# Kernel tuning notes

Hardware: AMD Instinct MI355X
Metric: run time of the kernel (lower is better)

Reference implementation:

```python
import jax, jax.numpy as jnp
import numpy as np

N_NODES = 100000


def _sage_conv(x, src, dst, Wl, Wr, b):
    # PyG SAGEConv (aggr='mean'): out = lin_l(mean_j x_j) + lin_r(x_i)
    deg = jax.ops.segment_sum(jnp.ones_like(src, dtype=x.dtype), dst, num_segments=N_NODES)
    agg = jax.ops.segment_sum(x[src], dst, num_segments=N_NODES)
    agg = agg / jnp.clip(deg, 1.0)[:, None]
    return agg @ Wl.T + x @ Wr.T + b


def setup_inputs() -> dict:
    key = jax.random.key(0)
    ks = jax.random.split(key, 16)
    N, E, ES = N_NODES, 1600000, 100000
    IN, H, D = 64, 128, 64

    def lin(k, out_c, in_c):
        s = 1.0 / np.sqrt(in_c)
        return jax.random.uniform(k, (out_c, in_c), jnp.float32, -s, s)

    inp = {
        "x": jax.random.normal(ks[0], (N, IN), jnp.float32),
        "edge_index": jax.random.randint(ks[1], (2, E), 0, N, jnp.int64),
        "edge_sample": jax.random.randint(ks[2], (2, ES), 0, N, jnp.int64),
        # SAGEConv 0: 64 -> 128
        "Wl0": lin(ks[3], H, IN), "Wr0": lin(ks[4], H, IN), "b0": jnp.zeros((H,), jnp.float32),
        # SAGEConv 1: 128 -> 128
        "Wl1": lin(ks[5], H, H), "Wr1": lin(ks[6], H, H), "b1": jnp.zeros((H,), jnp.float32),
        # SAGEConv 2: 128 -> 64
        "Wl2": lin(ks[7], D, H), "Wr2": lin(ks[8], D, H), "b2": jnp.zeros((D,), jnp.float32),
        # feature decoder MLP: 64 -> 128 -> 64
        "Wd1": lin(ks[9], H, D), "bd1": jnp.zeros((H,), jnp.float32),
        "Wd2": lin(ks[10], IN, H), "bd2": jnp.zeros((IN,), jnp.float32),
    }
    return inp


def reference(x, edge_index, edge_sample, Wl0, Wr0, b0, Wl1, Wr1, b1, Wl2, Wr2, b2, Wd1, bd1, Wd2, bd2):
    src, dst = edge_index[0], edge_index[1]
    # encoder (dropout = identity at inference)
    h = jax.nn.relu(_sage_conv(x, src, dst, Wl0, Wr0, b0))
    h = jax.nn.relu(_sage_conv(h, src, dst, Wl1, Wr1, b1))
    emb = _sage_conv(h, src, dst, Wl2, Wr2, b2)
    # feature decoder
    rec = jax.nn.relu(emb @ Wd1.T + bd1) @ Wd2.T + bd2
    # edge decoder: dot product
    edge_scores = jnp.sum(emb[edge_sample[0]] * emb[edge_sample[1]], axis=1)
    return emb, rec, edge_scores
```

## Files before the change

kernel.cpp:

```cpp
#include <hip/hip_runtime.h>

#define NN 100000
#define NBK 98
#define CHUNK 8192
typedef unsigned int uint;
typedef unsigned short ushort;

using f32x4 = __attribute__((ext_vector_type(4))) float;
using s16x8 = __attribute__((ext_vector_type(8))) short;

__device__ inline ushort f32_to_bf16(float f) {
  uint u = __float_as_uint(f);
  uint r = (u + 0x7FFFu + ((u >> 16) & 1u)) >> 16;
  return (ushort)r;
}
__device__ inline float bf16_to_f32(ushort h) {
  return __uint_as_float(((uint)h) << 16);
}

typedef __attribute__((address_space(1))) const unsigned int gas_u32;
typedef __attribute__((address_space(3))) unsigned int las_u32;
__device__ __forceinline__ void gld_lds16(const void* gp, void* lp) {
  __builtin_amdgcn_global_load_lds((gas_u32*)gp, (las_u32*)lp, 16, 0, 0);
}

struct P8 { const float* p[8]; };

__global__ void k_prep(const int* __restrict__ dst, uint* __restrict__ bcnt, int E, int NCB,
                       const float* __restrict__ x, ushort* __restrict__ xb, int n4, int NC,
                       P8 w, ushort* __restrict__ whi, int wtotal) {
  int b = blockIdx.x;
  int tid = threadIdx.x;
  if (b < NCB) {
    __shared__ uint hist[NBK];
    for (int i = tid; i < NBK; i += 256) hist[i] = 0;
    __syncthreads();
    int base = b * CHUNK;
    int lim = min(base + CHUNK, E);
    for (int e = base + tid; e < lim; e += 256) atomicAdd(&hist[(uint)dst[e] >> 10], 1u);
    __syncthreads();
    for (int i = tid; i < NBK; i += 256)
      if (hist[i]) atomicAdd(&bcnt[i], hist[i]);
  } else if (b < NCB + NC) {
    int i = (b - NCB) * 256 + tid;
    if (i < n4) {
      float4 v = ((const float4*)x)[i];
      uint2 o;
      o.x = (uint)f32_to_bf16(v.x) | ((uint)f32_to_bf16(v.y) << 16);
      o.y = (uint)f32_to_bf16(v.z) | ((uint)f32_to_bf16(v.w) << 16);
      ((uint2*)xb)[i] = o;
    }
  } else {
    int g = (b - NCB - NC) * 256 + tid;
    if (g < wtotal) {
      const int offs[8] = {0, 8192, 16384, 32768, 49152, 57344, 65536, 73728};
      int s = 0;
#pragma unroll
      for (int i = 1; i < 8; ++i) s += (g >= offs[i]);
      whi[g] = f32_to_bf16(w.p[s][g - offs[s]]);
    }
  }
}

__global__ void k_bscan(const uint* __restrict__ bcnt, uint* __restrict__ bbase,
                        uint* __restrict__ bcur, int* __restrict__ rp) {
  if (threadIdx.x == 0) {
    uint s = 0;
    for (int i = 0; i < NBK; ++i) {
      uint c = bcnt[i];
      bbase[i] = s;
      bcur[i] = s;
      s += c;
    }
    bbase[NBK] = s;
    rp[NN] = (int)s;
  }
}

__global__ void k_bscatter(const int* __restrict__ src, const int* __restrict__ dst,
                           uint* __restrict__ bcur, uint* __restrict__ packed, int E) {
  __shared__ uint hist[NBK], runbase[NBK], cur[NBK];
  int tid = threadIdx.x;
  for (int i = tid; i < NBK; i += 256) hist[i] = 0;
  __syncthreads();
  int base = blockIdx.x * CHUNK;
  int lim = min(base + CHUNK, E);
  for (int e = base + tid; e < lim; e += 256) atomicAdd(&hist[(uint)dst[e] >> 10], 1u);
  __syncthreads();
  for (int i = tid; i < NBK; i += 256) {
    runbase[i] = hist[i] ? atomicAdd(&bcur[i], hist[i]) : 0u;
    cur[i] = 0;
  }
  __syncthreads();
  for (int e = base + tid; e < lim; e += 256) {
    uint d = (uint)dst[e];
    uint s = (uint)src[e];
    uint bk = d >> 10;
    uint p = runbase[bk] + atomicAdd(&cur[bk], 1u);
    packed[p] = ((d & 1023u) << 20) | s;
  }
}

__global__ void k_build(const uint* __restrict__ bbase, const uint* __restrict__ packed,
                        int* __restrict__ rp, int* __restrict__ col) {
  __shared__ uint hist[1024];
  __shared__ uint ws[256];
  int b = blockIdx.x;
  int tid = threadIdx.x;
  uint lo = bbase[b], hi = bbase[b + 1];
#pragma unroll
  for (int i = 0; i < 4; ++i) hist[tid + i * 256] = 0;
  __syncthreads();
  for (uint e = lo + tid; e < hi; e += 256) atomicAdd(&hist[packed[e] >> 20], 1u);
  __syncthreads();
  uint v0 = hist[tid * 4], v1 = hist[tid * 4 + 1], v2 = hist[tid * 4 + 2], v3 = hist[tid * 4 + 3];
  ws[tid] = v0 + v1 + v2 + v3;
  __syncthreads();
  for (int off = 1; off < 256; off <<= 1) {
    uint add = (tid >= off) ? ws[tid - off] : 0u;
    __syncthreads();
    ws[tid] += add;
    __syncthreads();
  }
  uint ex = (tid > 0) ? ws[tid - 1] : 0u;
  hist[tid * 4] = ex;
  hist[tid * 4 + 1] = ex + v0;
  hist[tid * 4 + 2] = ex + v0 + v1;
  hist[tid * 4 + 3] = ex + v0 + v1 + v2;
  int nodeBase = b << 10;
#pragma unroll
  for (int i = 0; i < 4; ++i) {
    int node = nodeBase + tid * 4 + i;
    if (node < NN) rp[node] = (int)(lo + hist[tid * 4 + i]);
  }
  __syncthreads();
  for (uint e = lo + tid; e < hi; e += 256) {
    uint pk = packed[e];
    uint p = atomicAdd(&hist[pk >> 20], 1u);
    col[lo + p] = (int)(pk & 0xFFFFFu);
  }
}

#define ACC1(vv) { alo += __uint_as_float((vv) << 16); ahi += __uint_as_float((vv) & 0xffff0000u); }

template <int F, int MODE>
__global__ void k_agg(const ushort* __restrict__ x, const int* __restrict__ rp,
                      const int* __restrict__ col, const float* __restrict__ u,
                      float* __restrict__ of, ushort* __restrict__ ob, int n) {
  constexpr int RS = F / 2;
  int wave = (blockIdx.x * blockDim.x + threadIdx.x) >> 6;
  int lane = threadIdx.x & 63;
  int node, l;
  if (F == 128) { node = wave; l = lane; }
  else { node = wave * 2 + (lane >> 5); l = lane & 31; }
  if (node >= n) return;
  int beg = rp[node], end = rp[node + 1];
  int deg = end - beg;
  const uint* __restrict__ xu = (const uint*)x;
  float alo = 0.f, ahi = 0.f;
  int j = beg;
  for (; j + 8 <= end; j += 8) {
    int c0 = col[j], c1 = col[j + 1], c2 = col[j + 2], c3 = col[j + 3];
    int c4 = col[j + 4], c5 = col[j + 5], c6 = col[j + 6], c7 = col[j + 7];
    uint v0 = xu[(size_t)c0 * RS + l];
    uint v1 = xu[(size_t)c1 * RS + l];
    uint v2 = xu[(size_t)c2 * RS + l];
    uint v3 = xu[(size_t)c3 * RS + l];
    uint v4 = xu[(size_t)c4 * RS + l];
    uint v5 = xu[(size_t)c5 * RS + l];
    uint v6 = xu[(size_t)c6 * RS + l];
    uint v7 = xu[(size_t)c7 * RS + l];
    ACC1(v0) ACC1(v1) ACC1(v2) ACC1(v3) ACC1(v4) ACC1(v5) ACC1(v6) ACC1(v7)
  }
  if (j + 4 <= end) {
    int c0 = col[j], c1 = col[j + 1], c2 = col[j + 2], c3 = col[j + 3];
    uint v0 = xu[(size_t)c0 * RS + l];
    uint v1 = xu[(size_t)c1 * RS + l];
    uint v2 = xu[(size_t)c2 * RS + l];
    uint v3 = xu[(size_t)c3 * RS + l];
    ACC1(v0) ACC1(v1) ACC1(v2) ACC1(v3)
    j += 4;
  }
  for (; j < end; ++j) {
    uint v0 = xu[(size_t)col[j] * RS + l];
    ACC1(v0)
  }
  float inv = 1.0f / (float)(deg > 0 ? deg : 1);
  alo *= inv;
  ahi *= inv;
  if (MODE == 0) {
    ((uint*)ob)[(size_t)node * RS + l] = (uint)f32_to_bf16(alo) | ((uint)f32_to_bf16(ahi) << 16);
  } else {
    float2 uv = ((const float2*)u)[(size_t)node * RS + l];
    float e0 = alo + uv.x, e1 = ahi + uv.y;
    ((float2*)of)[(size_t)node * RS + l] = make_float2(e0, e1);
    ((uint*)ob)[(size_t)node * RS + l] = (uint)f32_to_bf16(e0) | ((uint)f32_to_bf16(e1) << 16);
  }
}

template <int K, int H, bool RELU, bool DUAL, int OUTM>
__global__ __launch_bounds__(256) void k_gemm(
    const ushort* __restrict__ A, const ushort* __restrict__ Wa,
    const ushort* __restrict__ B, const ushort* __restrict__ Wb,
    const float* __restrict__ bias,
    float* __restrict__ outf, ushort* __restrict__ outb, int n) {
  constexpr int BM = 128;
  constexpr int KT = 64;
  constexpr int NKT = K / KT;
  constexpr int MF = (H == 128) ? 4 : 2;
  constexpr int WCH = H / 32;
  __shared__ ushort As[BM * KT];
  __shared__ ushort Ws[H * KT];

  const int tid = threadIdx.x;
  const int lane = tid & 63;
  const int wid = tid >> 6;
  const int fr = lane & 15;
  const int fq = lane >> 4;
  const int blockRow = blockIdx.x * BM;
  const int rowBase = (H == 128) ? (wid >> 1) * 64 : wid * 32;
  const int colBase = (H == 128) ? (wid & 1) * 64 : 0;
  const int srow = lane >> 3;
  const int sslot = (lane & 7) ^ srow;
  const bool fullTile = (blockRow + BM <= n);

  f32x4 acc[MF][4];
#pragma unroll
  for (int mi = 0; mi < MF; ++mi)
#pragma unroll
    for (int ni = 0; ni < 4; ++ni) acc[mi][ni] = (f32x4){0.f, 0.f, 0.f, 0.f};

#pragma unroll
  for (int phase = 0; phase < (DUAL ? 2 : 1); ++phase) {
    const ushort* __restrict__ Ap = phase ? B : A;
    const ushort* __restrict__ Wp = phase ? Wb : Wa;
#pragma unroll
    for (int kt = 0; kt < NKT; ++kt) {
      const int ktb = kt * KT;
      __syncthreads();
      if (fullTile) {
#pragma unroll
        for (int i = 0; i < 4; ++i) {
          int r0 = (wid + i * 4) * 8;
          gld_lds16(Ap + (size_t)(blockRow + r0 + srow) * K + ktb + sslot * 8,
                    (char*)As + r0 * 128);
        }
#pragma unroll
        for (int i = 0; i < WCH; ++i) {
          int r0 = (wid + i * 4) * 8;
          if (WCH >= 4 || wid + i * 4 < WCH * 4)
            gld_lds16(Wp + (size_t)(r0 + srow) * K + ktb + sslot * 8,
                      (char*)Ws + r0 * 128);
        }
      } else {
        for (int c = tid; c < BM * 8; c += 256) {
          int r = c >> 3, kc = c & 7;
          int row = blockRow + r;
          uint4 v = make_uint4(0u, 0u, 0u, 0u);
          if (row < n) v = *(const uint4*)(Ap + (size_t)row * K + ktb + kc * 8);
          *(uint4*)((char*)As + r * 128 + ((kc * 16) ^ ((r & 7) << 4))) = v;
        }
        for (int c = tid; c < H * 8; c += 256) {
          int r = c >> 3, kc = c & 7;
          *(uint4*)((char*)Ws + r * 128 + ((kc * 16) ^ ((r & 7) << 4))) =
              *(const uint4*)(Wp + (size_t)r * K + ktb + kc * 8);
        }
      }
      __syncthreads();
#pragma unroll
      for (int ks = 0; ks < 2; ++ks) {
        const int kb = ks * 64 + fq * 16;
        s16x8 af[MF], wf[4];
#pragma unroll
        for (int mi = 0; mi < MF; ++mi) {
          int r = rowBase + mi * 16 + fr;
          af[mi] = *(const s16x8*)((const char*)As + r * 128 + (kb ^ ((r & 7) << 4)));
        }
#pragma unroll
        for (int ni = 0; ni < 4; ++ni) {
          int r = colBase + ni * 16 + fr;
          wf[ni] = *(const s16x8*)((const char*)Ws + r * 128 + (kb ^ ((r & 7) << 4)));
        }
#pragma unroll
        for (int mi = 0; mi < MF; ++mi)
#pragma unroll
          for (int ni = 0; ni < 4; ++ni)
            acc[mi][ni] = __builtin_amdgcn_mfma_f32_16x16x32_bf16(af[mi], wf[ni], acc[mi][ni], 0, 0, 0);
      }
    }
  }
#pragma unroll
  for (int mi = 0; mi < MF; ++mi) {
#pragma unroll
    for (int ni = 0; ni < 4; ++ni) {
#pragma unroll
      for (int r = 0; r < 4; ++r) {
        int row = blockRow + rowBase + mi * 16 + fq * 4 + r;
        int colI = colBase + ni * 16 + fr;
        if (row < n) {
          float v = acc[mi][ni][r];
          if (OUTM == 3) {
            if (colI < 64)
              outb[(size_t)row * 64 + colI] = f32_to_bf16(v);
            else
              outf[(size_t)row * 64 + (colI - 64)] = v + bias[colI - 64];
          } else {
            if (bias) v += bias[colI];
            if (RELU) v = fmaxf(v, 0.f);
            if (OUTM == 1) outf[(size_t)row * H + colI] = v;
            else outb[(size_t)row * H + colI] = f32_to_bf16(v);
          }
        }
      }
    }
  }
}

__global__ void k_dot(const float* __restrict__ emb, const int* __restrict__ ea,
                      const int* __restrict__ eb, float* __restrict__ out, int ne) {
  int hw = (blockIdx.x * blockDim.x + threadIdx.x) >> 5;
  int l = threadIdx.x & 31;
  if (hw >= ne) return;
  float2 a = ((const float2*)(emb + (size_t)ea[hw] * 64))[l];
  float2 b = ((const float2*)(emb + (size_t)eb[hw] * 64))[l];
  float v = a.x * b.x + a.y * b.y;
#pragma unroll
  for (int off = 16; off; off >>= 1) v += __shfl_xor(v, off, 64);
  if (l == 0) out[hw] = v;
}

extern "C" void kernel_launch(void* const* d_in, const int* in_sizes, int n_in,
                              void* d_out, int out_size, void* d_ws, size_t ws_size,
                              hipStream_t stream) {
  const float* x = (const float*)d_in[0];
  const int* ei = (const int*)d_in[1];
  const int* es = (const int*)d_in[2];
  const float* b0 = (const float*)d_in[5];
  const float* b1 = (const float*)d_in[8];
  const float* b2 = (const float*)d_in[11];
  const float* bd1 = (const float*)d_in[13];
  const float* bd2 = (const float*)d_in[15];

  const int E = in_sizes[1] / 2;
  const int ES = in_sizes[2] / 2;
  const int* srcv = ei;
  const int* dstv = ei + E;
  const int* ea = es;
  const int* eb = es + ES;

  char* wp = (char*)d_ws;
  auto alloc = [&](size_t bytes) {
    char* p = wp;
    wp += (bytes + 511) & ~(size_t)511;
    return p;
  };
  int* row_ptr = (int*)alloc((NN + 1) * sizeof(int));
  uint* bcnt = (uint*)alloc(NBK * sizeof(uint));
  uint* bbase = (uint*)alloc((NBK + 1) * sizeof(uint));
  uint* bcur = (uint*)alloc(NBK * sizeof(uint));
  uint* packed = (uint*)alloc((size_t)E * sizeof(uint));
  int* colv = (int*)alloc((size_t)E * sizeof(int));
  ushort* xb = (ushort*)alloc((size_t)NN * 64 * 2);
  ushort* aggb = (ushort*)alloc((size_t)NN * 128 * 2);
  ushort* h1b = (ushort*)alloc((size_t)NN * 128 * 2);
  ushort* h2b = (ushort*)alloc((size_t)NN * 128 * 2);
  float* uf = (float*)alloc((size_t)NN * 64 * 4);
  ushort* embb = (ushort*)alloc((size_t)NN * 64 * 2);
  ushort* Whb = (ushort*)alloc(81920 * 2);

  const int WO0 = 0, WO1 = 8192, WO2 = 16384, WO3 = 32768, WO4 = 49152,
            WO6 = 65536, WO7 = 73728;

  float* out_emb = (float*)d_out;
  float* out_rec = out_emb + (size_t)NN * 64;
  float* out_sc = out_rec + (size_t)NN * 64;

  hipMemsetAsync(bcnt, 0, NBK * sizeof(uint), stream);

  P8 wptrs;
  wptrs.p[0] = (const float*)d_in[3];  wptrs.p[1] = (const float*)d_in[4];
  wptrs.p[2] = (const float*)d_in[6];  wptrs.p[3] = (const float*)d_in[7];
  wptrs.p[4] = (const float*)d_in[9];  wptrs.p[5] = (const float*)d_in[10];
  wptrs.p[6] = (const float*)d_in[12]; wptrs.p[7] = (const float*)d_in[14];

  const int NCB = (E + CHUNK - 1) / CHUNK;
  const int n4 = NN * 64 / 4;
  const int NC = (n4 + 255) / 256;
  const int NS = (81920 + 255) / 256;
  k_prep<<<NCB + NC + NS, 256, 0, stream>>>(dstv, bcnt, E, NCB, x, xb, n4, NC,
                                            wptrs, Whb, 81920);
  k_bscan<<<1, 64, 0, stream>>>(bcnt, bbase, bcur, row_ptr);
  k_bscatter<<<NCB, 256, 0, stream>>>(srcv, dstv, bcur, packed, E);
  k_build<<<NBK, 256, 0, stream>>>(bbase, packed, row_ptr, colv);

  const int g64 = (NN + 7) / 8;
  const int g128a = (NN + 3) / 4;
  dim3 gg((NN + 127) / 128);

  k_agg<64, 0><<<g64, 256, 0, stream>>>(xb, row_ptr, colv, nullptr, nullptr, aggb, NN);
  k_gemm<64, 128, true, true, 0><<<gg, 256, 0, stream>>>(
      aggb, Whb + WO0, xb, Whb + WO1, b0, nullptr, h1b, NN);
  k_agg<128, 0><<<g128a, 256, 0, stream>>>(h1b, row_ptr, colv, nullptr, nullptr, aggb, NN);
  k_gemm<128, 128, true, true, 0><<<gg, 256, 0, stream>>>(
      aggb, Whb + WO2, h1b, Whb + WO3, b1, nullptr, h2b, NN);
  k_gemm<128, 128, false, false, 3><<<gg, 256, 0, stream>>>(
      h2b, Whb + WO4, nullptr, nullptr, b2, uf, aggb, NN);
  k_agg<64, 2><<<g64, 256, 0, stream>>>(aggb, row_ptr, colv, uf, out_emb, embb, NN);
  k_gemm<64, 128, true, false, 0><<<gg, 256, 0, stream>>>(
      embb, Whb + WO6, nullptr, nullptr, bd1, nullptr, h1b, NN);
  k_gemm<128, 64, false, false, 1><<<gg, 256, 0, stream>>>(
      h1b, Whb + WO7, nullptr, nullptr, bd2, out_rec, nullptr, NN);
  k_dot<<<(ES + 7) / 8, 256, 0, stream>>>(out_emb, ea, eb, out_sc, ES);
}
```

Before: 366.6 us.

## Fuse decoder MLP, load full-K GEMM tiles, precompute per-chunk scatter offsets

Three changes. The two decoder GEMMs are merged into one kernel that keeps the 128-wide hidden activation in LDS, so it is never written to and reread from global memory. The GEMM kernel now loads the whole K extent of A and W into LDS at once instead of looping over 64-wide K tiles, which removes per-tile barriers but uses more LDS per block. The bucket scatter reuses per-chunk histograms from the prep kernel plus a per-bucket scan, so it no longer recomputes histograms or issues global atomics; the cost is a serial scan over chunks in a single block.

```diff
diff --git a/kernel.cpp b/kernel.cpp
--- a/kernel.cpp
+++ b/kernel.cpp
@@ -26,7 +26,8 @@
 
 struct P8 { const float* p[8]; };
 
-__global__ void k_prep(const int* __restrict__ dst, uint* __restrict__ bcnt, int E, int NCB,
+__global__ void k_prep(const int* __restrict__ dst, uint* __restrict__ bcnt,
+                       uint* __restrict__ chunkCnt, int E, int NCB,
                        const float* __restrict__ x, ushort* __restrict__ xb, int n4, int NC,
                        P8 w, ushort* __restrict__ whi, int wtotal) {
   int b = blockIdx.x;
@@ -39,8 +40,11 @@
     int lim = min(base + CHUNK, E);
     for (int e = base + tid; e < lim; e += 256) atomicAdd(&hist[(uint)dst[e] >> 10], 1u);
     __syncthreads();
-    for (int i = tid; i < NBK; i += 256)
-      if (hist[i]) atomicAdd(&bcnt[i], hist[i]);
+    for (int i = tid; i < NBK; i += 256) {
+      uint h = hist[i];
+      chunkCnt[(size_t)b * NBK + i] = h;
+      if (h) atomicAdd(&bcnt[i], h);
+    }
   } else if (b < NCB + NC) {
     int i = (b - NCB) * 256 + tid;
     if (i < n4) {
@@ -63,40 +67,45 @@
 }
 
 __global__ void k_bscan(const uint* __restrict__ bcnt, uint* __restrict__ bbase,
-                        uint* __restrict__ bcur, int* __restrict__ rp) {
+                        int* __restrict__ rp, const uint* __restrict__ chunkCnt,
+                        uint* __restrict__ chunkBase, int NCB) {
+  __shared__ uint sbase[NBK + 1];
   if (threadIdx.x == 0) {
     uint s = 0;
     for (int i = 0; i < NBK; ++i) {
-      uint c = bcnt[i];
-      bbase[i] = s;
-      bcur[i] = s;
-      s += c;
-    }
-    bbase[NBK] = s;
+      sbase[i] = s;
+      s += bcnt[i];
+    }
+    sbase[NBK] = s;
     rp[NN] = (int)s;
+    for (int i = 0; i <= NBK; ++i) bbase[i] = sbase[i];
+  }
+  __syncthreads();
+  int bk = threadIdx.x;
+  if (bk < NBK) {
+    uint run = sbase[bk];
+    for (int c = 0; c < NCB; ++c) {
+      uint v = chunkCnt[(size_t)c * NBK + bk];
+      chunkBase[(size_t)c * NBK + bk] = run;
+      run += v;
+    }
   }
 }
 
 __global__ void k_bscatter(const int* __restrict__ src, const int* __restrict__ dst,
-                           uint* __restrict__ bcur, uint* __restrict__ packed, int E) {
-  __shared__ uint hist[NBK], runbase[NBK], cur[NBK];
+                           const uint* __restrict__ chunkBase, uint* __restrict__ packed, int E) {
+  __shared__ uint cur[NBK];
   int tid = threadIdx.x;
-  for (int i = tid; i < NBK; i += 256) hist[i] = 0;
-  __syncthreads();
-  int base = blockIdx.x * CHUNK;
+  int b = blockIdx.x;
+  for (int i = tid; i < NBK; i += 256) cur[i] = chunkBase[(size_t)b * NBK + i];
+  __syncthreads();
+  int base = b * CHUNK;
   int lim = min(base + CHUNK, E);
-  for (int e = base + tid; e < lim; e += 256) atomicAdd(&hist[(uint)dst[e] >> 10], 1u);
-  __syncthreads();
-  for (int i = tid; i < NBK; i += 256) {
-    runbase[i] = hist[i] ? atomicAdd(&bcur[i], hist[i]) : 0u;
-    cur[i] = 0;
-  }
-  __syncthreads();
   for (int e = base + tid; e < lim; e += 256) {
     uint d = (uint)dst[e];
     uint s = (uint)src[e];
     uint bk = d >> 10;
-    uint p = runbase[bk] + atomicAdd(&cur[bk], 1u);
+    uint p = atomicAdd(&cur[bk], 1u);
     packed[p] = ((d & 1023u) << 20) | s;
   }
 }
@@ -205,12 +214,14 @@
     const float* __restrict__ bias,
     float* __restrict__ outf, ushort* __restrict__ outb, int n) {
   constexpr int BM = 128;
-  constexpr int KT = 64;
-  constexpr int NKT = K / KT;
   constexpr int MF = (H == 128) ? 4 : 2;
-  constexpr int WCH = H / 32;
-  __shared__ ushort As[BM * KT];
-  __shared__ ushort Ws[H * KT];
+  constexpr int RB = 2 * K;
+  constexpr int SLOTS = K / 8;
+  constexpr int CR = 1024 / RB;
+  constexpr int ACH = BM * RB / 1024;
+  constexpr int WCHN = H * RB / 1024;
+  __shared__ ushort As[BM * K];
+  __shared__ ushort Ws[H * K];
 
   const int tid = threadIdx.x;
   const int lane = tid & 63;
@@ -220,8 +231,8 @@
   const int blockRow = blockIdx.x * BM;
   const int rowBase = (H == 128) ? (wid >> 1) * 64 : wid * 32;
   const int colBase = (H == 128) ? (wid & 1) * 64 : 0;
-  const int srow = lane >> 3;
-  const int sslot = (lane & 7) ^ srow;
+  const int srow = lane / SLOTS;
+  const int sl = lane % SLOTS;
   const bool fullTile = (blockRow + BM <= n);
 
   f32x4 acc[MF][4];
@@ -234,59 +245,54 @@
   for (int phase = 0; phase < (DUAL ? 2 : 1); ++phase) {
     const ushort* __restrict__ Ap = phase ? B : A;
     const ushort* __restrict__ Wp = phase ? Wb : Wa;
-#pragma unroll
-    for (int kt = 0; kt < NKT; ++kt) {
-      const int ktb = kt * KT;
-      __syncthreads();
-      if (fullTile) {
-#pragma unroll
-        for (int i = 0; i < 4; ++i) {
-          int r0 = (wid + i * 4) * 8;
-          gld_lds16(Ap + (size_t)(blockRow + r0 + srow) * K + ktb + sslot * 8,
-                    (char*)As + r0 * 128);
-        }
-#pragma unroll
-        for (int i = 0; i < WCH; ++i) {
-          int r0 = (wid + i * 4) * 8;
-          if (WCH >= 4 || wid + i * 4 < WCH * 4)
-            gld_lds16(Wp + (size_t)(r0 + srow) * K + ktb + sslot * 8,
-                      (char*)Ws + r0 * 128);
-        }
-      } else {
-        for (int c = tid; c < BM * 8; c += 256) {
-          int r = c >> 3, kc = c & 7;
-          int row = blockRow + r;
-          uint4 v = make_uint4(0u, 0u, 0u, 0u);
-          if (row < n) v = *(const uint4*)(Ap + (size_t)row * K + ktb + kc * 8);
-          *(uint4*)((char*)As + r * 128 + ((kc * 16) ^ ((r & 7) << 4))) = v;
-        }
-        for (int c = tid; c < H * 8; c += 256) {
-          int r = c >> 3, kc = c & 7;
-          *(uint4*)((char*)Ws + r * 128 + ((kc * 16) ^ ((r & 7) << 4))) =
-              *(const uint4*)(Wp + (size_t)r * K + ktb + kc * 8);
-        }
-      }
-      __syncthreads();
-#pragma unroll
-      for (int ks = 0; ks < 2; ++ks) {
-        const int kb = ks * 64 + fq * 16;
-        s16x8 af[MF], wf[4];
-#pragma unroll
-        for (int mi = 0; mi < MF; ++mi) {
-          int r = rowBase + mi * 16 + fr;
-          af[mi] = *(const s16x8*)((const char*)As + r * 128 + (kb ^ ((r & 7) << 4)));
-        }
-#pragma unroll
-        for (int ni = 0; ni < 4; ++ni) {
-          int r = colBase + ni * 16 + fr;
-          wf[ni] = *(const s16x8*)((const char*)Ws + r * 128 + (kb ^ ((r & 7) << 4)));
-        }
-#pragma unroll
-        for (int mi = 0; mi < MF; ++mi)
-#pragma unroll
-          for (int ni = 0; ni < 4; ++ni)
-            acc[mi][ni] = __builtin_amdgcn_mfma_f32_16x16x32_bf16(af[mi], wf[ni], acc[mi][ni], 0, 0, 0);
-      }
+    if (phase) __syncthreads();
+    if (fullTile) {
+#pragma unroll
+      for (int i = 0; i < ACH / 4; ++i) {
+        int r0 = (wid + i * 4) * CR;
+        int grow = r0 + srow;
+        gld_lds16(Ap + (size_t)(blockRow + grow) * K + (sl ^ (grow & 7)) * 8,
+                  (char*)As + r0 * RB);
+      }
+#pragma unroll
+      for (int i = 0; i < WCHN / 4; ++i) {
+        int r0 = (wid + i * 4) * CR;
+        int grow = r0 + srow;
+        gld_lds16(Wp + (size_t)grow * K + (sl ^ (grow & 7)) * 8, (char*)Ws + r0 * RB);
+      }
+    } else {
+      for (int c = tid; c < BM * SLOTS; c += 256) {
+        int r = c / SLOTS, s = c % SLOTS;
+        int row = blockRow + r;
+        uint4 v = make_uint4(0u, 0u, 0u, 0u);
+        if (row < n) v = *(const uint4*)(Ap + (size_t)row * K + s * 8);
+        *(uint4*)((char*)As + r * RB + ((s ^ (r & 7)) << 4)) = v;
+      }
+      for (int c = tid; c < H * SLOTS; c += 256) {
+        int r = c / SLOTS, s = c % SLOTS;
+        *(uint4*)((char*)Ws + r * RB + ((s ^ (r & 7)) << 4)) =
+            *(const uint4*)(Wp + (size_t)r * K + s * 8);
+      }
+    }
+    __syncthreads();
+#pragma unroll
+    for (int ks = 0; ks < K / 32; ++ks) {
+      s16x8 af[MF], wf[4];
+#pragma unroll
+      for (int mi = 0; mi < MF; ++mi) {
+        int r = rowBase + mi * 16 + fr;
+        af[mi] = *(const s16x8*)((const char*)As + r * RB + (((ks * 4 + fq) ^ (r & 7)) << 4));
+      }
+#pragma unroll
+      for (int ni = 0; ni < 4; ++ni) {
+        int r = colBase + ni * 16 + fr;
+        wf[ni] = *(const s16x8*)((const char*)Ws + r * RB + (((ks * 4 + fq) ^ (r & 7)) << 4));
+      }
+#pragma unroll
+      for (int mi = 0; mi < MF; ++mi)
+#pragma unroll
+        for (int ni = 0; ni < 4; ++ni)
+          acc[mi][ni] = __builtin_amdgcn_mfma_f32_16x16x32_bf16(af[mi], wf[ni], acc[mi][ni], 0, 0, 0);
     }
   }
 #pragma unroll
@@ -316,6 +322,144 @@
   }
 }
 
+__global__ __launch_bounds__(256) void k_dec(
+    const ushort* __restrict__ emb, const ushort* __restrict__ Wd1,
+    const float* __restrict__ bd1, const ushort* __restrict__ Wd2,
+    const float* __restrict__ bd2, float* __restrict__ rec, int n) {
+  __shared__ ushort As[128 * 64];
+  __shared__ ushort W1[128 * 64];
+  __shared__ ushort Hs[128 * 128];
+  __shared__ ushort W2[64 * 128];
+
+  const int tid = threadIdx.x;
+  const int lane = tid & 63;
+  const int wid = tid >> 6;
+  const int fr = lane & 15;
+  const int fq = lane >> 4;
+  const int blockRow = blockIdx.x * 128;
+  const int rowBase1 = (wid >> 1) * 64;
+  const int colBase1 = (wid & 1) * 64;
+  const int srow8 = lane >> 3, sl8 = lane & 7;
+  const int srow4 = lane >> 4, sl16 = lane & 15;
+  const bool fullTile = (blockRow + 128 <= n);
+
+  if (fullTile) {
+#pragma unroll
+    for (int i = 0; i < 4; ++i) {
+      int r0 = (wid + i * 4) * 8;
+      gld_lds16(emb + (size_t)(blockRow + r0 + srow8) * 64 + (sl8 ^ srow8) * 8,
+                (char*)As + r0 * 128);
+    }
+#pragma unroll
+    for (int i = 0; i < 4; ++i) {
+      int r0 = (wid + i * 4) * 8;
+      gld_lds16(Wd1 + (size_t)(r0 + srow8) * 64 + (sl8 ^ srow8) * 8, (char*)W1 + r0 * 128);
+    }
+#pragma unroll
+    for (int i = 0; i < 4; ++i) {
+      int r0 = (wid + i * 4) * 4;
+      int grow = r0 + srow4;
+      gld_lds16(Wd2 + (size_t)grow * 128 + (sl16 ^ (grow & 7)) * 8, (char*)W2 + r0 * 256);
+    }
+  } else {
+    for (int c = tid; c < 128 * 8; c += 256) {
+      int r = c >> 3, s = c & 7;
+      int row = blockRow + r;
+      uint4 v = make_uint4(0u, 0u, 0u, 0u);
+      if (row < n) v = *(const uint4*)(emb + (size_t)row * 64 + s * 8);
+      *(uint4*)((char*)As + r * 128 + ((s ^ (r & 7)) << 4)) = v;
+    }
+    for (int c = tid; c < 128 * 8; c += 256) {
+      int r = c >> 3, s = c & 7;
+      *(uint4*)((char*)W1 + r * 128 + ((s ^ (r & 7)) << 4)) =
+          *(const uint4*)(Wd1 + (size_t)r * 64 + s * 8);
+    }
+    for (int c = tid; c < 64 * 16; c += 256) {
+      int r = c >> 4, s = c & 15;
+      *(uint4*)((char*)W2 + r * 256 + ((s ^ (r & 7)) << 4)) =
+          *(const uint4*)(Wd2 + (size_t)r * 128 + s * 8);
+    }
+  }
+  __syncthreads();
+
+  f32x4 a1[4][4];
+#pragma unroll
+  for (int mi = 0; mi < 4; ++mi)
+#pragma unroll
+    for (int ni = 0; ni < 4; ++ni) a1[mi][ni] = (f32x4){0.f, 0.f, 0.f, 0.f};
+#pragma unroll
+  for (int ks = 0; ks < 2; ++ks) {
+    s16x8 af[4], wf[4];
+#pragma unroll
+    for (int mi = 0; mi < 4; ++mi) {
+      int r = rowBase1 + mi * 16 + fr;
+      af[mi] = *(const s16x8*)((const char*)As + r * 128 + (((ks * 4 + fq) ^ (r & 7)) << 4));
+    }
+#pragma unroll
+    for (int ni = 0; ni < 4; ++ni) {
+      int r = colBase1 + ni * 16 + fr;
+      wf[ni] = *(const s16x8*)((const char*)W1 + r * 128 + (((ks * 4 + fq) ^ (r & 7)) << 4));
+    }
+#pragma unroll
+    for (int mi = 0; mi < 4; ++mi)
+#pragma unroll
+      for (int ni = 0; ni < 4; ++ni)
+        a1[mi][ni] = __builtin_amdgcn_mfma_f32_16x16x32_bf16(af[mi], wf[ni], a1[mi][ni], 0, 0, 0);
+  }
+#pragma unroll
+  for (int mi = 0; mi < 4; ++mi) {
+#pragma unroll
+    for (int ni = 0; ni < 4; ++ni) {
+#pragma unroll
+      for (int r = 0; r < 4; ++r) {
+        int rowl = rowBase1 + mi * 16 + fq * 4 + r;
+        int colI = colBase1 + ni * 16 + fr;
+        float v = fmaxf(a1[mi][ni][r] + bd1[colI], 0.f);
+        int byte = rowl * 256 + ((((colI >> 3) ^ (rowl & 7))) << 4) + (colI & 7) * 2;
+        *(ushort*)((char*)Hs + byte) = f32_to_bf16(v);
+      }
+    }
+  }
+  __syncthreads();
+
+  f32x4 a2[2][4];
+#pragma unroll
+  for (int mi = 0; mi < 2; ++mi)
+#pragma unroll
+    for (int ni = 0; ni < 4; ++ni) a2[mi][ni] = (f32x4){0.f, 0.f, 0.f, 0.f};
+#pragma unroll
+  for (int kk = 0; kk < 4; ++kk) {
+    s16x8 af[2], wf[4];
+#pragma unroll
+    for (int mi = 0; mi < 2; ++mi) {
+      int r = wid * 32 + mi * 16 + fr;
+      af[mi] = *(const s16x8*)((const char*)Hs + r * 256 + (((kk * 4 + fq) ^ (r & 7)) << 4));
+    }
+#pragma unroll
+    for (int ni = 0; ni < 4; ++ni) {
+      int r = ni * 16 + fr;
+      wf[ni] = *(const s16x8*)((const char*)W2 + r * 256 + (((kk * 4 + fq) ^ (r & 7)) << 4));
+    }
+#pragma unroll
+    for (int mi = 0; mi < 2; ++mi)
+#pragma unroll
+      for (int ni = 0; ni < 4; ++ni)
+        a2[mi][ni] = __builtin_amdgcn_mfma_f32_16x16x32_bf16(af[mi], wf[ni], a2[mi][ni], 0, 0, 0);
+  }
+#pragma unroll
+  for (int mi = 0; mi < 2; ++mi) {
+#pragma unroll
+    for (int ni = 0; ni < 4; ++ni) {
+#pragma unroll
+      for (int r = 0; r < 4; ++r) {
+        int row = blockRow + wid * 32 + mi * 16 + fq * 4 + r;
+        int colI = ni * 16 + fr;
+        if (row < n) rec[(size_t)row * 64 + colI] = a2[mi][ni][r] + bd2[colI];
+      }
+    }
+  }
+}
+
 __global__ void k_dot(const float* __restrict__ emb, const int* __restrict__ ea,
                       const int* __restrict__ eb, float* __restrict__ out, int ne) {
   int hw = (blockIdx.x * blockDim.x + threadIdx.x) >> 5;
@@ -354,10 +498,12 @@
     wp += (bytes + 511) & ~(size_t)511;
     return p;
   };
+  const int NCB = (E + CHUNK - 1) / CHUNK;
   int* row_ptr = (int*)alloc((NN + 1) * sizeof(int));
   uint* bcnt = (uint*)alloc(NBK * sizeof(uint));
   uint* bbase = (uint*)alloc((NBK + 1) * sizeof(uint));
-  uint* bcur = (uint*)alloc(NBK * sizeof(uint));
+  uint* chunkCnt = (uint*)alloc((size_t)NCB * NBK * sizeof(uint));
+  uint* chunkBase = (uint*)alloc((size_t)NCB * NBK * sizeof(uint));
   uint* packed = (uint*)alloc((size_t)E * sizeof(uint));
   int* colv = (int*)alloc((size_t)E * sizeof(int));
   ushort* xb = (ushort*)alloc((size_t)NN * 64 * 2);
@@ -383,14 +529,13 @@
   wptrs.p[4] = (const float*)d_in[9];  wptrs.p[5] = (const float*)d_in[10];
   wptrs.p[6] = (const float*)d_in[12]; wptrs.p[7] = (const float*)d_in[14];
 
-  const int NCB = (E + CHUNK - 1) / CHUNK;
   const int n4 = NN * 64 / 4;
   const int NC = (n4 + 255) / 256;
   const int NS = (81920 + 255) / 256;
-  k_prep<<<NCB + NC + NS, 256, 0, stream>>>(dstv, bcnt, E, NCB, x, xb, n4, NC,
+  k_prep<<<NCB + NC + NS, 256, 0, stream>>>(dstv, bcnt, chunkCnt, E, NCB, x, xb, n4, NC,
                                             wptrs, Whb, 81920);
-  k_bscan<<<1, 64, 0, stream>>>(bcnt, bbase, bcur, row_ptr);
-  k_bscatter<<<NCB, 256, 0, stream>>>(srcv, dstv, bcur, packed, E);
+  k_bscan<<<1, 256, 0, stream>>>(bcnt, bbase, row_ptr, chunkCnt, chunkBase, NCB);
+  k_bscatter<<<NCB, 256, 0, stream>>>(srcv, dstv, chunkBase, packed, E);
   k_build<<<NBK, 256, 0, stream>>>(bbase, packed, row_ptr, colv);
 
   const int g64 = (NN + 7) / 8;
@@ -406,9 +551,6 @@
   k_gemm<128, 128, false, false, 3><<<gg, 256, 0, stream>>>(
       h2b, Whb + WO4, nullptr, nullptr, b2, uf, aggb, NN);
   k_agg<64, 2><<<g64, 256, 0, stream>>>(aggb, row_ptr, colv, uf, out_emb, embb, NN);
-  k_gemm<64, 128, true, false, 0><<<gg, 256, 0, stream>>>(
-      embb, Whb + WO6, nullptr, nullptr, bd1, nullptr, h1b, NN);
-  k_gemm<128, 64, false, false, 1><<<gg, 256, 0, stream>>>(
-      h1b, Whb + WO7, nullptr, nullptr, bd2, out_rec, nullptr, NN);
+  k_dec<<<gg, 256, 0, stream>>>(embb, Whb + WO6, bd1, Whb + WO7, bd2, out_rec, NN);
   k_dot<<<(ES + 7) / 8, 256, 0, stream>>>(out_emb, ea, eb, out_sc, ES);
 }
```

New measurement: 388.5 us. 6.0% more time.
